# Kernel tuning notes

Measured on AMD Instinct MI355X. Metric: run time of the kernel, lower is better.

Reference implementation:

```python
import jax, jax.numpy as jnp
import numpy as np

B, T, C = 1, 4096, 1024
H = 16
D = C // H  # 64
LN_EPS = 1e-5


def layer_norm(x, g, b):
    mu = jnp.mean(x, axis=-1, keepdims=True)
    var = jnp.mean(jnp.square(x - mu), axis=-1, keepdims=True)
    return (x - mu) * jax.lax.rsqrt(var + LN_EPS) * g + b


def setup_inputs() -> dict:
    key = jax.random.key(0)
    ks = jax.random.split(key, 8)
    s = 0.02
    return {
        "x": jax.random.normal(ks[0], (B, T, C), dtype=jnp.float32),
        "ln1_g": jnp.ones((C,), jnp.float32),
        "ln1_b": jnp.zeros((C,), jnp.float32),
        "Wqkv": jax.random.normal(ks[1], (C, 3 * C), dtype=jnp.float32) * s,
        "bqkv": jnp.zeros((3 * C,), jnp.float32),
        "Wo": jax.random.normal(ks[2], (C, C), dtype=jnp.float32) * s,
        "bo": jnp.zeros((C,), jnp.float32),
        "ln2_g": jnp.ones((C,), jnp.float32),
        "ln2_b": jnp.zeros((C,), jnp.float32),
        "W1": jax.random.normal(ks[3], (C, 4 * C), dtype=jnp.float32) * s,
        "b1": jnp.zeros((4 * C,), jnp.float32),
        "W2": jax.random.normal(ks[4], (4 * C, C), dtype=jnp.float32) * s,
        "b2": jnp.zeros((C,), jnp.float32),
    }


def reference(x, ln1_g, ln1_b, Wqkv, bqkv, Wo, bo, ln2_g, ln2_b, W1, b1, W2, b2):
    b, t, c = x.shape
    x_norm = layer_norm(x, ln1_g, ln1_b)
    qkv = x_norm @ Wqkv + bqkv                      # [B,T,3C]
    qkv = qkv.reshape(b, t, 3, H, D).transpose(2, 0, 3, 1, 4)  # [3,B,H,T,D]
    Q, K, V = qkv[0], qkv[1], qkv[2]
    scores = jnp.einsum("bhtd,bhsd->bhts", Q, K) / jnp.sqrt(jnp.float32(D))
    causal = jnp.tril(jnp.ones((t, t), dtype=bool))  # [T,T]
    scores = jnp.where(causal[None, None], scores, -jnp.inf)
    weights = jax.nn.softmax(scores, axis=-1)
    attn = jnp.einsum("bhts,bhsd->bhtd", weights, V)  # [B,H,T,D]
    attn = attn.transpose(0, 2, 1, 3).reshape(b, t, c)
    x = x + (attn @ Wo + bo)
    h = layer_norm(x, ln2_g, ln2_b)
    h = jax.nn.gelu(h @ W1 + b1, approximate=False) @ W2 + b2
    return x + h
```

## Files before the change

kernel.cpp:

```cpp
#include <hip/hip_runtime.h>
#include <math.h>

typedef __bf16 bf16_t;
typedef __attribute__((ext_vector_type(8))) __bf16 bf16x8;
typedef __attribute__((ext_vector_type(4))) __bf16 bf16x4;
typedef __attribute__((ext_vector_type(4))) float f32x4;
typedef __attribute__((ext_vector_type(16))) float f32x16;
typedef __attribute__((ext_vector_type(4))) unsigned int u32x4;

#define T_LEN 4096
#define C_DIM 1024
#define NH 16
#define HD 64

__device__ __forceinline__ void gload_lds16(const void* g, void* l) {
    __builtin_amdgcn_global_load_lds(
        (__attribute__((address_space(1))) void*)(g),
        (__attribute__((address_space(3))) void*)(l), 16, 0, 0);
}

__device__ __forceinline__ f32x4 mfma16(bf16x8 a, bf16x8 b, f32x4 c) {
    return __builtin_amdgcn_mfma_f32_16x16x32_bf16(a, b, c, 0, 0, 0);
}

__device__ __forceinline__ f32x16 mfma32(bf16x8 a, bf16x8 b, f32x16 c) {
    return __builtin_amdgcn_mfma_f32_32x32x16_bf16(a, b, c, 0, 0, 0);
}

__device__ __forceinline__ float gelu_exact(float v) {
    return 0.5f * v * (1.0f + erff(v * 0.7071067811865476f));
}

__device__ __forceinline__ void make_frags2(const f32x16 s, bf16x8& fx, bf16x8& fy) {
    unsigned a0, a1, b0, b1;
    asm("v_cvt_pk_bf16_f32 %0, %1, %2" : "=v"(a0) : "v"(s[0]), "v"(s[1]));
    asm("v_cvt_pk_bf16_f32 %0, %1, %2" : "=v"(a1) : "v"(s[2]), "v"(s[3]));
    asm("v_cvt_pk_bf16_f32 %0, %1, %2" : "=v"(b0) : "v"(s[4]), "v"(s[5]));
    asm("v_cvt_pk_bf16_f32 %0, %1, %2" : "=v"(b1) : "v"(s[6]), "v"(s[7]));
    asm("v_permlane32_swap_b32 %0, %1" : "+v"(a0), "+v"(b0));
    asm("v_permlane32_swap_b32 %0, %1" : "+v"(a1), "+v"(b1));
    u32x4 wa = {a0, a1, b0, b1};
    fx = __builtin_bit_cast(bf16x8, wa);
    unsigned c0, c1, d0, d1;
    asm("v_cvt_pk_bf16_f32 %0, %1, %2" : "=v"(c0) : "v"(s[8]), "v"(s[9]));
    asm("v_cvt_pk_bf16_f32 %0, %1, %2" : "=v"(c1) : "v"(s[10]), "v"(s[11]));
    asm("v_cvt_pk_bf16_f32 %0, %1, %2" : "=v"(d0) : "v"(s[12]), "v"(s[13]));
    asm("v_cvt_pk_bf16_f32 %0, %1, %2" : "=v"(d1) : "v"(s[14]), "v"(s[15]));
    asm("v_permlane32_swap_b32 %0, %1" : "+v"(c0), "+v"(d0));
    asm("v_permlane32_swap_b32 %0, %1" : "+v"(c1), "+v"(d1));
    u32x4 wb = {c0, c1, d0, d1};
    fy = __builtin_bit_cast(bf16x8, wb);
}

__global__ __launch_bounds__(256) void transpose_all(
    const float* __restrict__ wqkv, const float* __restrict__ wo,
    const float* __restrict__ w1, const float* __restrict__ w2,
    bf16_t* __restrict__ oqkv, bf16_t* __restrict__ owo,
    bf16_t* __restrict__ ow1, bf16_t* __restrict__ ow2)
{
    __shared__ float tile[32][33];
    int s = blockIdx.x;
    const float* in; bf16_t* out; int R, C, NBX;
    if (s < 3072)      {            in = wqkv; out = oqkv; R = 1024; C = 3072; NBX = 96; }
    else if (s < 4096) { s -= 3072; in = wo;   out = owo;  R = 1024; C = 1024; NBX = 32; }
    else if (s < 8192) { s -= 4096; in = w1;   out = ow1;  R = 1024; C = 4096; NBX = 128; }
    else               { s -= 8192; in = w2;   out = ow2;  R = 4096; C = 1024; NBX = 32; }
    const int tx = threadIdx.x, ty = threadIdx.y;
    const int c0 = (s % NBX) * 32, r0 = (s / NBX) * 32;
#pragma unroll
    for (int j = 0; j < 4; ++j)
        tile[ty + j * 8][tx] = in[(size_t)(r0 + ty + j * 8) * C + c0 + tx];
    __syncthreads();
#pragma unroll
    for (int j = 0; j < 4; ++j)
        out[(size_t)(c0 + ty + j * 8) * R + r0 + tx] = (bf16_t)tile[tx][ty + j * 8];
}

__global__ __launch_bounds__(256) void ln_bf16(
    const float* __restrict__ x, const float* __restrict__ gam,
    const float* __restrict__ bet, bf16_t* __restrict__ out)
{
    const int row = blockIdx.x, t = threadIdx.x;
    const float4 v = *(const float4*)(x + (size_t)row * 1024 + t * 4);
    float s1 = v.x + v.y + v.z + v.w;
    float s2 = v.x * v.x + v.y * v.y + v.z * v.z + v.w * v.w;
#pragma unroll
    for (int m = 1; m < 64; m <<= 1) {
        s1 += __shfl_xor(s1, m);
        s2 += __shfl_xor(s2, m);
    }
    __shared__ float red[8];
    if ((t & 63) == 0) { red[(t >> 6) * 2] = s1; red[(t >> 6) * 2 + 1] = s2; }
    __syncthreads();
    s1 = red[0] + red[2] + red[4] + red[6];
    s2 = red[1] + red[3] + red[5] + red[7];
    const float mu = s1 * (1.0f / 1024.0f);
    const float inv = rsqrtf(s2 * (1.0f / 1024.0f) - mu * mu + 1e-5f);
    const float4 gg = *(const float4*)(gam + t * 4);
    const float4 bb = *(const float4*)(bet + t * 4);
    bf16x4 o;
    o[0] = (bf16_t)((v.x - mu) * inv * gg.x + bb.x);
    o[1] = (bf16_t)((v.y - mu) * inv * gg.y + bb.y);
    o[2] = (bf16_t)((v.z - mu) * inv * gg.z + bb.z);
    o[3] = (bf16_t)((v.w - mu) * inv * gg.w + bb.w);
    *(bf16x4*)(out + (size_t)row * 1024 + t * 4) = o;
}

template <int EPI>
__global__ __launch_bounds__(256, 2) void gemm_bt(
    const bf16_t* __restrict__ A, const bf16_t* __restrict__ Bt,
    const float* __restrict__ bias, const float* __restrict__ res,
    bf16_t* __restrict__ outb, float* __restrict__ outf,
    int M, int N, int Klen, int Kstr)
{
    __shared__ alignas(1024) bf16_t Alds[4][128 * 32];
    __shared__ alignas(1024) bf16_t Blds[4][128 * 32];
    const int t = threadIdx.x;
    const int lane = t & 63, w = t >> 6;
    const int wr = w >> 1, wc = w & 1;
    const int g = lane >> 4, ci = lane & 15;

    const int NB = gridDim.x, MB = gridDim.y;
    const int flat = blockIdx.x + NB * blockIdx.y;
    const int xcd = flat & 7, slot = flat >> 3;
    const int by = xcd * (MB >> 3) + slot / NB;
    const int bx = slot % NB;
    const int m0 = by * 128, n0 = bx * 128;

    f32x4 acc[4][4];
#pragma unroll
    for (int i = 0; i < 4; ++i)
#pragma unroll
        for (int j = 0; j < 4; ++j)
#pragma unroll
            for (int k = 0; k < 4; ++k) acc[i][j][k] = 0.0f;

    const int r0 = t >> 2;
    const int cc = (t & 3) * 8;
    const int nkt = Klen >> 5;

    auto stage = [&](int kt) {
        const int b = kt & 3;
        const int kk = kt * 32;
        char* aB = (char*)&Alds[b][0] + w * 1024;
        char* bB = (char*)&Blds[b][0] + w * 1024;
        gload_lds16(A + (size_t)(m0 + r0) * Kstr + kk + cc, aB);
        gload_lds16(A + (size_t)(m0 + r0 + 64) * Kstr + kk + cc, aB + 4096);
        gload_lds16(Bt + (size_t)(n0 + r0) * Kstr + kk + cc, bB);
        gload_lds16(Bt + (size_t)(n0 + r0 + 64) * Kstr + kk + cc, bB + 4096);
    };

    stage(0);
    if (nkt > 1) stage(1);
    for (int kt = 0; kt < nkt; ++kt) {
        if (kt + 2 < nkt) {
            stage(kt + 2);
            asm volatile("s_waitcnt vmcnt(8)" ::: "memory");
        } else if (kt + 1 < nkt) {
            asm volatile("s_waitcnt vmcnt(4)" ::: "memory");
        } else {
            asm volatile("s_waitcnt vmcnt(0)" ::: "memory");
        }
        __builtin_amdgcn_s_barrier();
        __builtin_amdgcn_sched_barrier(0);
        const int b = kt & 3;
        const bf16_t* ap = &Alds[b][0] + (wr * 64 + ci) * 32 + g * 8;
        const bf16_t* bp = &Blds[b][0] + (wc * 64 + ci) * 32 + g * 8;
        bf16x8 af[4], bf[4];
#pragma unroll
        for (int mt = 0; mt < 4; ++mt) af[mt] = *(const bf16x8*)(ap + mt * 16 * 32);
#pragma unroll
        for (int nt = 0; nt < 4; ++nt) bf[nt] = *(const bf16x8*)(bp + nt * 16 * 32);
        __builtin_amdgcn_s_setprio(1);
#pragma unroll
        for (int mt = 0; mt < 4; ++mt)
#pragma unroll
            for (int nt = 0; nt < 4; ++nt)
                acc[mt][nt] = mfma16(af[mt], bf[nt], acc[mt][nt]);
        __builtin_amdgcn_s_setprio(0);
    }

#pragma unroll
    for (int nt = 0; nt < 4; ++nt) {
        const int col = n0 + wc * 64 + nt * 16 + ci;
        const float bv = bias[col];
#pragma unroll
        for (int mt = 0; mt < 4; ++mt) {
            const int row = m0 + wr * 64 + mt * 16 + g * 4;
#pragma unroll
            for (int r = 0; r < 4; ++r) {
                float v = acc[mt][nt][r] + bv;
                if constexpr (EPI == 1) v = gelu_exact(v);
                if constexpr (EPI == 2) {
                    outf[(size_t)(row + r) * N + col] =
                        v + res[(size_t)(row + r) * N + col];
                } else {
                    outb[(size_t)(row + r) * N + col] = (bf16_t)v;
                }
            }
        }
    }
}

__global__ __launch_bounds__(512, 1) void gemm_w2(
    const bf16_t* __restrict__ A, const bf16_t* __restrict__ Bt,
    const float* __restrict__ bias, const float* __restrict__ res,
    float* __restrict__ out, int M, int N, int Khalf, int Kstr)
{
    __shared__ alignas(1024) char smem[131072];
    bf16_t* ring = (bf16_t*)smem;
    const int t = threadIdx.x;
    const int grp = t >> 8, tl = t & 255;
    const int lane = tl & 63, w = tl >> 6;
    const int wr = w >> 1, wc = w & 1;
    const int g = lane >> 4, ci = lane & 15;

    const int NB = gridDim.x, MB = gridDim.y;
    const int flat = blockIdx.x + NB * blockIdx.y;
    const int xcd = flat & 7, slot = flat >> 3;
    const int by = xcd * (MB >> 3) + slot / NB;
    const int bx = slot % NB;
    const int m0 = by * 128, n0 = bx * 128;

    const bf16_t* Ag = A + (size_t)grp * Khalf;
    const bf16_t* Bg = Bt + (size_t)grp * Khalf;

    f32x4 acc[4][4];
#pragma unroll
    for (int i = 0; i < 4; ++i)
#pragma unroll
        for (int j = 0; j < 4; ++j)
#pragma unroll
            for (int k = 0; k < 4; ++k) acc[i][j][k] = 0.0f;

    const int r0 = tl >> 2;
    const int cc = (tl & 3) * 8;
    const int nkt = Khalf >> 5;

    auto stage = [&](int kt) {
        const int b = kt & 3;
        const int kk = kt * 32;
        bf16_t* base = ring + grp * 32768 + b * 8192;
        char* aB = (char*)base + w * 1024;
        char* bB = (char*)(base + 4096) + w * 1024;
        gload_lds16(Ag + (size_t)(m0 + r0) * Kstr + kk + cc, aB);
        gload_lds16(Ag + (size_t)(m0 + r0 + 64) * Kstr + kk + cc, aB + 4096);
        gload_lds16(Bg + (size_t)(n0 + r0) * Kstr + kk + cc, bB);
        gload_lds16(Bg + (size_t)(n0 + r0 + 64) * Kstr + kk + cc, bB + 4096);
    };

    stage(0);
    stage(1);
    for (int kt = 0; kt < nkt; ++kt) {
        if (kt + 2 < nkt) {
            stage(kt + 2);
            asm volatile("s_waitcnt vmcnt(8)" ::: "memory");
        } else if (kt + 1 < nkt) {
            asm volatile("s_waitcnt vmcnt(4)" ::: "memory");
        } else {
            asm volatile("s_waitcnt vmcnt(0)" ::: "memory");
        }
        __builtin_amdgcn_s_barrier();
        __builtin_amdgcn_sched_barrier(0);
        const bf16_t* base = ring + grp * 32768 + (kt & 3) * 8192;
        const bf16_t* ap = base + (wr * 64 + ci) * 32 + g * 8;
        const bf16_t* bp = base + 4096 + (wc * 64 + ci) * 32 + g * 8;
        bf16x8 af[4], bf[4];
#pragma unroll
        for (int mt = 0; mt < 4; ++mt) af[mt] = *(const bf16x8*)(ap + mt * 16 * 32);
#pragma unroll
        for (int nt = 0; nt < 4; ++nt) bf[nt] = *(const bf16x8*)(bp + nt * 16 * 32);
        __builtin_amdgcn_s_setprio(1);
#pragma unroll
        for (int mt = 0; mt < 4; ++mt)
#pragma unroll
            for (int nt = 0; nt < 4; ++nt)
                acc[mt][nt] = mfma16(af[mt], bf[nt], acc[mt][nt]);
        __builtin_amdgcn_s_setprio(0);
    }

    __syncthreads();
    float* ex = (float*)smem;
    if (grp == 1) {
#pragma unroll
        for (int mt = 0; mt < 4; ++mt)
#pragma unroll
            for (int nt = 0; nt < 4; ++nt)
                *(f32x4*)(ex + tl * 68 + (mt * 4 + nt) * 4) = acc[mt][nt];
    }
    __syncthreads();
    if (grp == 0) {
#pragma unroll
        for (int nt = 0; nt < 4; ++nt) {
            const int col = n0 + wc * 64 + nt * 16 + ci;
            const float bv = bias[col];
#pragma unroll
            for (int mt = 0; mt < 4; ++mt) {
                const int row = m0 + wr * 64 + mt * 16 + g * 4;
                const f32x4 p1 = *(const f32x4*)(ex + tl * 68 + (mt * 4 + nt) * 4);
#pragma unroll
                for (int r = 0; r < 4; ++r) {
                    out[(size_t)(row + r) * N + col] =
                        acc[mt][nt][r] + p1[r] + bv +
                        res[(size_t)(row + r) * N + col];
                }
            }
        }
    }
}

template <int EPI>
__global__ __launch_bounds__(512, 2) void gemm256(
    const bf16_t* __restrict__ A, const bf16_t* __restrict__ Bt,
    const float* __restrict__ bias, bf16_t* __restrict__ outb,
    bf16_t* __restrict__ vtout, int M, int N, int K)
{
    __shared__ alignas(1024) bf16_t lds[2][2][256 * 64];
    const int t = threadIdx.x, lane = t & 63, w = t >> 6;
    const int g = lane >> 4, ci = lane & 15;
    const int wr = w >> 2, wc = w & 3;
    const int NB = gridDim.x;
    const int nwg = NB * gridDim.y;
    const int flat = blockIdx.x + NB * blockIdx.y;
    const int rix = (flat & 7) * (nwg >> 3) + (flat >> 3);
    const int m0 = (rix / NB) * 256, n0 = (rix % NB) * 256;
    const int NKT = K >> 6;

    f32x4 acc[8][4];
#pragma unroll
    for (int i = 0; i < 8; ++i)
#pragma unroll
        for (int j = 0; j < 4; ++j)
#pragma unroll
            for (int k2 = 0; k2 < 4; ++k2) acc[i][j][k2] = 0.0f;

    const int sw0 = (g ^ (ci & 7)) * 8;
    const int sw1 = ((4 + g) ^ (ci & 7)) * 8;

    auto stage = [&](int h, int ktile, int b) {
#pragma unroll
        for (int i = 0; i < 2; ++i) {
            const int idx = i * 512 + t;
            const int r = idx >> 3;
            const int c = (t & 7) ^ (r & 7);
            const bf16_t* src = ((h < 2) ? A : Bt)
                + (size_t)(((h < 2) ? m0 : n0) + (h & 1) * 128 + r) * K
                + ktile * 64 + c * 8;
            bf16_t* dst = &lds[b][h >> 1][(h & 1) * 8192] + (i * 512 + w * 64) * 8;
            gload_lds16(src, dst);
        }
    };

    bf16x8 a[4][2], b2[2][2][2];

    stage(0, 0, 0); stage(3, 0, 0); stage(1, 0, 0); stage(2, 0, 0);
    if (NKT > 1) { stage(0, 1, 1); stage(3, 1, 1); stage(1, 1, 1); }
    asm volatile("s_waitcnt vmcnt(6)" ::: "memory");
    __builtin_amdgcn_s_barrier();

    for (int kt = 0; kt < NKT; ++kt) {
        const int cur = kt & 1;
        const bf16_t* Ab = &lds[cur][0][0];
        const bf16_t* Bb = &lds[cur][1][0];

#pragma unroll
        for (int mi = 0; mi < 4; ++mi) {
            const bf16_t* ap = Ab + (wr * 64 + mi * 16 + ci) * 64;
            a[mi][0] = *(const bf16x8*)(ap + sw0);
            a[mi][1] = *(const bf16x8*)(ap + sw1);
        }
#pragma unroll
        for (int ni = 0; ni < 2; ++ni) {
            const bf16_t* bp = Bb + (wc * 32 + ni * 16 + ci) * 64;
            b2[0][ni][0] = *(const bf16x8*)(bp + sw0);
            b2[0][ni][1] = *(const bf16x8*)(bp + sw1);
        }
        if (kt + 1 < NKT) stage(2, kt + 1, cur ^ 1);
        __builtin_amdgcn_s_barrier();
        asm volatile("s_waitcnt lgkmcnt(0)" ::: "memory");
        __builtin_amdgcn_sched_barrier(0);
        __builtin_amdgcn_s_setprio(1);
#pragma unroll
        for (int mi = 0; mi < 4; ++mi)
#pragma unroll
            for (int ni = 0; ni < 2; ++ni) {
                acc[mi][ni] = mfma16(a[mi][0], b2[0][ni][0], acc[mi][ni]);
                acc[mi][ni] = mfma16(a[mi][1], b2[0][ni][1], acc[mi][ni]);
            }
        __builtin_amdgcn_s_setprio(0);
        __builtin_amdgcn_s_barrier();

#pragma unroll
        for (int ni = 0; ni < 2; ++ni) {
            const bf16_t* bp = Bb + (128 + wc * 32 + ni * 16 + ci) * 64;
            b2[1][ni][0] = *(const bf16x8*)(bp + sw0);
            b2[1][ni][1] = *(const bf16x8*)(bp + sw1);
        }
        if (kt + 2 < NKT) stage(0, kt + 2, cur);
        __builtin_amdgcn_s_barrier();
        asm volatile("s_waitcnt lgkmcnt(0)" ::: "memory");
        __builtin_amdgcn_sched_barrier(0);
        __builtin_amdgcn_s_setprio(1);
#pragma unroll
        for (int mi = 0; mi < 4; ++mi)
#pragma unroll
            for (int ni = 0; ni < 2; ++ni) {
                acc[mi][2 + ni] = mfma16(a[mi][0], b2[1][ni][0], acc[mi][2 + ni]);
                acc[mi][2 + ni] = mfma16(a[mi][1], b2[1][ni][1], acc[mi][2 + ni]);
            }
        __builtin_amdgcn_s_setprio(0);
        __builtin_amdgcn_s_barrier();

#pragma unroll
        for (int mi = 0; mi < 4; ++mi) {
            const bf16_t* ap = Ab + (128 + wr * 64 + mi * 16 + ci) * 64;
            a[mi][0] = *(const bf16x8*)(ap + sw0);
            a[mi][1] = *(const bf16x8*)(ap + sw1);
        }
        if (kt + 2 < NKT) stage(3, kt + 2, cur);
        __builtin_amdgcn_s_barrier();
        asm volatile("s_waitcnt lgkmcnt(0)" ::: "memory");
        __builtin_amdgcn_sched_barrier(0);
        __builtin_amdgcn_s_setprio(1);
#pragma unroll
        for (int mi = 0; mi < 4; ++mi)
#pragma unroll
            for (int ni = 0; ni < 2; ++ni) {
                acc[4 + mi][2 + ni] = mfma16(a[mi][0], b2[1][ni][0], acc[4 + mi][2 + ni]);
                acc[4 + mi][2 + ni] = mfma16(a[mi][1], b2[1][ni][1], acc[4 + mi][2 + ni]);
            }
        __builtin_amdgcn_s_setprio(0);
        __builtin_amdgcn_s_barrier();

        if (kt + 2 < NKT) stage(1, kt + 2, cur);
        __builtin_amdgcn_s_barrier();
        __builtin_amdgcn_s_setprio(1);
#pragma unroll
        for (int mi = 0; mi < 4; ++mi)
#pragma unroll
            for (int ni = 0; ni < 2; ++ni) {
                acc[4 + mi][ni] = mfma16(a[mi][0], b2[0][ni][0], acc[4 + mi][ni]);
                acc[4 + mi][ni] = mfma16(a[mi][1], b2[0][ni][1], acc[4 + mi][ni]);
            }
        __builtin_amdgcn_s_setprio(0);
        if (kt + 2 < NKT) asm volatile("s_waitcnt vmcnt(6)" ::: "memory");
        else              asm volatile("s_waitcnt vmcnt(0)" ::: "memory");
        __builtin_amdgcn_s_barrier();
    }

    const float QSC = 0.125f * 1.4426950408889634f;
#pragma unroll
    for (int mrep = 0; mrep < 8; ++mrep) {
        const int row = m0 + (mrep >> 2) * 128 + wr * 64 + (mrep & 3) * 16 + g * 4;
#pragma unroll
        for (int nrep = 0; nrep < 4; ++nrep) {
            const int col = n0 + (nrep >> 1) * 128 + wc * 32 + (nrep & 1) * 16 + ci;
            const float bv = bias[col];
            if (EPI == 2 && col >= 2048) {
                const int cv = col - 2048;
                bf16x4 o4;
#pragma unroll
                for (int jr = 0; jr < 4; ++jr)
                    o4[jr] = (bf16_t)(acc[mrep][nrep][jr] + bv);
                *(bf16x4*)(vtout + (size_t)(cv >> 6) * 262144
                           + (size_t)(cv & 63) * 4096 + row) = o4;
            } else {
                const float sc = (EPI == 2 && col < 1024) ? QSC : 1.0f;
#pragma unroll
                for (int jr = 0; jr < 4; ++jr) {
                    float v = acc[mrep][nrep][jr] + bv;
                    if constexpr (EPI == 1) v = gelu_exact(v);
                    if (EPI == 2) v *= sc;
                    outb[(size_t)(row + jr) * N + col] = (bf16_t)v;
                }
            }
        }
    }
}

__global__ __launch_bounds__(256, 2) void attn_fwd(
    const bf16_t* __restrict__ qkv, const bf16_t* __restrict__ vt,
    bf16_t* __restrict__ opart, float* __restrict__ lbuf)
{
    __shared__ alignas(1024) bf16_t Klds[2][64 * 64];
    __shared__ alignas(1024) bf16_t Vlds[2][64 * 64];
    const int t = threadIdx.x, lane = t & 63, w = t >> 6;
    const int hi = lane >> 5, li = lane & 31;
    const int lq = li >> 2;
    const int h = blockIdx.x;
    const int y = blockIdx.y;
    const int qt = 31 - (y >> 1);
    const int chunk = y & 1;
    const int q0 = qt * 128;
    const int qrow = q0 + w * 32 + li;
    const int wDiag = 2 * qt + (w >> 1);
    const int ktA = chunk ? (qt + 1) : 0;
    const int ktB = chunk ? (2 * qt + 2) : (qt + 1);

    bf16x8 qf[4];
#pragma unroll
    for (int ks = 0; ks < 4; ++ks)
        qf[ks] = *(const bf16x8*)(qkv + (size_t)qrow * 3072 + h * 64 + ks * 16 + hi * 8);
    bf16x8 ones8;
#pragma unroll
    for (int j = 0; j < 8; ++j) ones8[j] = (bf16_t)1.0f;

    f32x16 oacc[2], lacc;
#pragma unroll
    for (int r = 0; r < 16; ++r) { oacc[0][r] = 0.0f; oacc[1][r] = 0.0f; lacc[r] = 0.0f; }

    const int sr = t >> 3;
    const int sx = ((t & 7) ^ ((sr >> 2) & 7)) * 8;

    auto stageKV = [&](int kt, int b) {
        const size_t kbase = (size_t)(kt * 64) * 3072 + 1024 + h * 64 + sx;
        const size_t vbase = (size_t)h * 262144 + (size_t)kt * 64 + sx;
#pragma unroll
        for (int i = 0; i < 2; ++i) {
            gload_lds16(qkv + kbase + (size_t)(i * 32 + sr) * 3072,
                        (char*)&Klds[b][0] + (size_t)(i * 2048 + t * 8) * 2);
            gload_lds16(vt + vbase + (size_t)(i * 32 + sr) * 4096,
                        (char*)&Vlds[b][0] + (size_t)(i * 2048 + t * 8) * 2);
        }
    };

    stageKV(ktA, 0);
    for (int kt = ktA; kt < ktB; ++kt) {
        const int cur = (kt - ktA) & 1;
        asm volatile("s_waitcnt vmcnt(0)" ::: "memory");
        __syncthreads();
        if (kt + 1 < ktB) stageKV(kt + 1, cur ^ 1);

        if (kt <= wDiag) {
            const bf16_t* Kb = &Klds[cur][0];
            const bf16_t* Vb = &Vlds[cur][0];
            f32x16 s0, s1;
#pragma unroll
            for (int r = 0; r < 16; ++r) { s0[r] = 0.0f; s1[r] = 0.0f; }

            __builtin_amdgcn_s_setprio(1);
#pragma unroll
            for (int ks = 0; ks < 4; ++ks) {
                const int cs = ((ks * 2 + hi) ^ lq) * 8;
                s0 = mfma32(*(const bf16x8*)(Kb + li * 64 + cs), qf[ks], s0);
                s1 = mfma32(*(const bf16x8*)(Kb + (32 + li) * 64 + cs), qf[ks], s1);
            }
            __builtin_amdgcn_s_setprio(0);

            bf16x8 vf[4][2];
#pragma unroll
            for (int ks = 0; ks < 4; ++ks) {
                const int cs = ((ks * 2 + hi) ^ lq) * 8;
                vf[ks][0] = *(const bf16x8*)(Vb + li * 64 + cs);
                vf[ks][1] = *(const bf16x8*)(Vb + (32 + li) * 64 + cs);
            }

            if (kt == wDiag) {
                const int kb0 = kt * 64 + 4 * hi;
#pragma unroll
                for (int r = 0; r < 16; ++r) {
                    const int kp0 = kb0 + (r & 3) + 8 * (r >> 2);
                    if (kp0 > qrow) s0[r] = -1e30f;
                    if (kp0 + 32 > qrow) s1[r] = -1e30f;
                }
            }
#pragma unroll
            for (int r = 0; r < 16; ++r) {
                s0[r] = exp2f(s0[r]);
                s1[r] = exp2f(s1[r]);
            }

            bf16x8 pf[4];
            make_frags2(s0, pf[0], pf[1]);
            make_frags2(s1, pf[2], pf[3]);

            __builtin_amdgcn_s_setprio(1);
#pragma unroll
            for (int ks = 0; ks < 4; ++ks) {
                oacc[0] = mfma32(vf[ks][0], pf[ks], oacc[0]);
                oacc[1] = mfma32(vf[ks][1], pf[ks], oacc[1]);
                lacc    = mfma32(ones8,     pf[ks], lacc);
            }
            __builtin_amdgcn_s_setprio(0);
        }
        __syncthreads();
    }

    bf16_t* op = opart + ((size_t)chunk * T_LEN + qrow) * 1024 + h * 64 + hi * 4;
#pragma unroll
    for (int dblk = 0; dblk < 2; ++dblk)
#pragma unroll
        for (int gi = 0; gi < 4; ++gi) {
            bf16x4 o4;
#pragma unroll
            for (int j = 0; j < 4; ++j) o4[j] = (bf16_t)oacc[dblk][gi * 4 + j];
            *(bf16x4*)(op + dblk * 32 + gi * 8) = o4;
        }
    if (hi == 0)
        lbuf[((size_t)chunk * T_LEN + qrow) * NH + h] = lacc[0];
}

__global__ __launch_bounds__(256) void attn_combine(
    const bf16_t* __restrict__ opart, const float* __restrict__ lbuf,
    bf16_t* __restrict__ out)
{
    const int row = blockIdx.x, t = threadIdx.x;
    const int c = t * 4, h = c >> 6;
    const float l0 = lbuf[(size_t)row * NH + h];
    const float l1 = lbuf[((size_t)T_LEN + row) * NH + h];
    const float inv = 1.0f / (l0 + l1);
    const bf16x4 o0 = *(const bf16x4*)(opart + (size_t)row * 1024 + c);
    const bf16x4 o1 = *(const bf16x4*)(opart + ((size_t)T_LEN + row) * 1024 + c);
    bf16x4 o;
#pragma unroll
    for (int j = 0; j < 4; ++j)
        o[j] = (bf16_t)(((float)o0[j] + (float)o1[j]) * inv);
    *(bf16x4*)(out + (size_t)row * 1024 + c) = o;
}

extern "C" void kernel_launch(void* const* d_in, const int* in_sizes, int n_in,
                              void* d_out, int out_size, void* d_ws, size_t ws_size,
                              hipStream_t stream)
{
    const float* x    = (const float*)d_in[0];
    const float* ln1g = (const float*)d_in[1];
    const float* ln1b = (const float*)d_in[2];
    const float* Wqkv = (const float*)d_in[3];
    const float* bqkv = (const float*)d_in[4];
    const float* Wo   = (const float*)d_in[5];
    const float* bo   = (const float*)d_in[6];
    const float* ln2g = (const float*)d_in[7];
    const float* ln2b = (const float*)d_in[8];
    const float* W1   = (const float*)d_in[9];
    const float* b1   = (const float*)d_in[10];
    const float* W2   = (const float*)d_in[11];
    const float* b2   = (const float*)d_in[12];
    float* outp = (float*)d_out;

    char* p = (char*)d_ws;
    bf16_t* WqkvT = (bf16_t*)p; p += (size_t)3072 * 1024 * 2;
    bf16_t* WoT   = (bf16_t*)p; p += (size_t)1024 * 1024 * 2;
    bf16_t* W1T   = (bf16_t*)p; p += (size_t)4096 * 1024 * 2;
    bf16_t* W2T   = (bf16_t*)p; p += (size_t)1024 * 4096 * 2;
    bf16_t* xn    = (bf16_t*)p; p += (size_t)4096 * 1024 * 2;
    bf16_t* qkv   = (bf16_t*)p; p += (size_t)4096 * 3072 * 2;
    bf16_t* vtb   = (bf16_t*)p; p += (size_t)16 * 64 * 4096 * 2;
    bf16_t* attnb = (bf16_t*)p; p += (size_t)4096 * 1024 * 2;
    float*  x2    = (float*)p;  p += (size_t)4096 * 1024 * 4;
    bf16_t* hb    = (bf16_t*)p; p += (size_t)4096 * 1024 * 2;
    bf16_t* g1    = (bf16_t*)p; p += (size_t)4096 * 4096 * 2;
    bf16_t* opart = (bf16_t*)p; p += (size_t)2 * 4096 * 1024 * 2;
    float*  lbuf  = (float*)p;  p += (size_t)2 * 4096 * 16 * 4;

    transpose_all<<<12288, dim3(32, 8), 0, stream>>>(Wqkv, Wo, W1, W2,
                                                     WqkvT, WoT, W1T, W2T);

    ln_bf16<<<4096, 256, 0, stream>>>(x, ln1g, ln1b, xn);
    gemm256<2><<<dim3(12, 16), 512, 0, stream>>>(xn, WqkvT, bqkv,
                                                 qkv, vtb, 4096, 3072, 1024);
    attn_fwd<<<dim3(16, 64), 256, 0, stream>>>(qkv, vtb, opart, lbuf);
    attn_combine<<<4096, 256, 0, stream>>>(opart, lbuf, attnb);
    gemm_bt<2><<<dim3(8, 32), 256, 0, stream>>>(attnb, WoT, bo, x,
                                                nullptr, x2, 4096, 1024, 1024, 1024);
    ln_bf16<<<4096, 256, 0, stream>>>(x2, ln2g, ln2b, hb);
    gemm256<1><<<dim3(16, 16), 512, 0, stream>>>(hb, W1T, b1,
                                                 g1, nullptr, 4096, 4096, 1024);
    gemm_w2<<<dim3(8, 32), 512, 0, stream>>>(g1, W2T, b2, x2,
                                             outp, 4096, 1024, 2048, 4096);
}
```

Baseline: 246.1 us.

## Use 256-row query tiles with four KV chunks and route Wo GEMM through split-K kernel

```diff
diff --git a/kernel.cpp b/kernel.cpp
--- a/kernel.cpp
+++ b/kernel.cpp
@@ -106,102 +106,6 @@
     *(bf16x4*)(out + (size_t)row * 1024 + t * 4) = o;
 }
 
-template <int EPI>
-__global__ __launch_bounds__(256, 2) void gemm_bt(
-    const bf16_t* __restrict__ A, const bf16_t* __restrict__ Bt,
-    const float* __restrict__ bias, const float* __restrict__ res,
-    bf16_t* __restrict__ outb, float* __restrict__ outf,
-    int M, int N, int Klen, int Kstr)
-{
-    __shared__ alignas(1024) bf16_t Alds[4][128 * 32];
-    __shared__ alignas(1024) bf16_t Blds[4][128 * 32];
-    const int t = threadIdx.x;
-    const int lane = t & 63, w = t >> 6;
-    const int wr = w >> 1, wc = w & 1;
-    const int g = lane >> 4, ci = lane & 15;
-
-    const int NB = gridDim.x, MB = gridDim.y;
-    const int flat = blockIdx.x + NB * blockIdx.y;
-    const int xcd = flat & 7, slot = flat >> 3;
-    const int by = xcd * (MB >> 3) + slot / NB;
-    const int bx = slot % NB;
-    const int m0 = by * 128, n0 = bx * 128;
-
-    f32x4 acc[4][4];
-#pragma unroll
-    for (int i = 0; i < 4; ++i)
-#pragma unroll
-        for (int j = 0; j < 4; ++j)
-#pragma unroll
-            for (int k = 0; k < 4; ++k) acc[i][j][k] = 0.0f;
-
-    const int r0 = t >> 2;
-    const int cc = (t & 3) * 8;
-    const int nkt = Klen >> 5;
-
-    auto stage = [&](int kt) {
-        const int b = kt & 3;
-        const int kk = kt * 32;
-        char* aB = (char*)&Alds[b][0] + w * 1024;
-        char* bB = (char*)&Blds[b][0] + w * 1024;
-        gload_lds16(A + (size_t)(m0 + r0) * Kstr + kk + cc, aB);
-        gload_lds16(A + (size_t)(m0 + r0 + 64) * Kstr + kk + cc, aB + 4096);
-        gload_lds16(Bt + (size_t)(n0 + r0) * Kstr + kk + cc, bB);
-        gload_lds16(Bt + (size_t)(n0 + r0 + 64) * Kstr + kk + cc, bB + 4096);
-    };
-
-    stage(0);
-    if (nkt > 1) stage(1);
-    for (int kt = 0; kt < nkt; ++kt) {
-        if (kt + 2 < nkt) {
-            stage(kt + 2);
-            asm volatile("s_waitcnt vmcnt(8)" ::: "memory");
-        } else if (kt + 1 < nkt) {
-            asm volatile("s_waitcnt vmcnt(4)" ::: "memory");
-        } else {
-            asm volatile("s_waitcnt vmcnt(0)" ::: "memory");
-        }
-        __builtin_amdgcn_s_barrier();
-        __builtin_amdgcn_sched_barrier(0);
-        const int b = kt & 3;
-        const bf16_t* ap = &Alds[b][0] + (wr * 64 + ci) * 32 + g * 8;
-        const bf16_t* bp = &Blds[b][0] + (wc * 64 + ci) * 32 + g * 8;
-        bf16x8 af[4], bf[4];
-#pragma unroll
-        for (int mt = 0; mt < 4; ++mt) af[mt] = *(const bf16x8*)(ap + mt * 16 * 32);
-#pragma unroll
-        for (int nt = 0; nt < 4; ++nt) bf[nt] = *(const bf16x8*)(bp + nt * 16 * 32);
-        __builtin_amdgcn_s_setprio(1);
-#pragma unroll
-        for (int mt = 0; mt < 4; ++mt)
-#pragma unroll
-            for (int nt = 0; nt < 4; ++nt)
-                acc[mt][nt] = mfma16(af[mt], bf[nt], acc[mt][nt]);
-        __builtin_amdgcn_s_setprio(0);
-    }
-
-#pragma unroll
-    for (int nt = 0; nt < 4; ++nt) {
-        const int col = n0 + wc * 64 + nt * 16 + ci;
-        const float bv = bias[col];
-#pragma unroll
-        for (int mt = 0; mt < 4; ++mt) {
-            const int row = m0 + wr * 64 + mt * 16 + g * 4;
-#pragma unroll
-            for (int r = 0; r < 4; ++r) {
-                float v = acc[mt][nt][r] + bv;
-                if constexpr (EPI == 1) v = gelu_exact(v);
-                if constexpr (EPI == 2) {
-                    outf[(size_t)(row + r) * N + col] =
-                        v + res[(size_t)(row + r) * N + col];
-                } else {
-                    outb[(size_t)(row + r) * N + col] = (bf16_t)v;
-                }
-            }
-        }
-    }
-}
-
 __global__ __launch_bounds__(512, 1) void gemm_w2(
     const bf16_t* __restrict__ A, const bf16_t* __restrict__ Bt,
     const float* __restrict__ bias, const float* __restrict__ res,
@@ -478,7 +382,7 @@
     }
 }
 
-__global__ __launch_bounds__(256, 2) void attn_fwd(
+__global__ __launch_bounds__(512, 2) void attn_fwd(
     const bf16_t* __restrict__ qkv, const bf16_t* __restrict__ vt,
     bf16_t* __restrict__ opart, float* __restrict__ lbuf)
 {
@@ -489,13 +393,13 @@
     const int lq = li >> 2;
     const int h = blockIdx.x;
     const int y = blockIdx.y;
-    const int qt = 31 - (y >> 1);
-    const int chunk = y & 1;
-    const int q0 = qt * 128;
+    const int qt = 15 - (y >> 2);
+    const int chunk = y & 3;
+    const int q0 = qt * 256;
     const int qrow = q0 + w * 32 + li;
-    const int wDiag = 2 * qt + (w >> 1);
-    const int ktA = chunk ? (qt + 1) : 0;
-    const int ktB = chunk ? (2 * qt + 2) : (qt + 1);
+    const int wDiag = 4 * qt + (w >> 1);
+    const int ktA = chunk * (qt + 1);
+    const int ktB = ktA + qt + 1;
 
     bf16x8 qf[4];
 #pragma unroll
@@ -513,15 +417,10 @@
     const int sx = ((t & 7) ^ ((sr >> 2) & 7)) * 8;
 
     auto stageKV = [&](int kt, int b) {
-        const size_t kbase = (size_t)(kt * 64) * 3072 + 1024 + h * 64 + sx;
-        const size_t vbase = (size_t)h * 262144 + (size_t)kt * 64 + sx;
-#pragma unroll
-        for (int i = 0; i < 2; ++i) {
-            gload_lds16(qkv + kbase + (size_t)(i * 32 + sr) * 3072,
-                        (char*)&Klds[b][0] + (size_t)(i * 2048 + t * 8) * 2);
-            gload_lds16(vt + vbase + (size_t)(i * 32 + sr) * 4096,
-                        (char*)&Vlds[b][0] + (size_t)(i * 2048 + t * 8) * 2);
-        }
+        gload_lds16(qkv + (size_t)(kt * 64 + sr) * 3072 + 1024 + h * 64 + sx,
+                    (char*)&Klds[b][0] + (size_t)t * 16);
+        gload_lds16(vt + (size_t)h * 262144 + (size_t)sr * 4096 + kt * 64 + sx,
+                    (char*)&Vlds[b][0] + (size_t)t * 16);
     };
 
     stageKV(ktA, 0);
@@ -606,15 +505,21 @@
 {
     const int row = blockIdx.x, t = threadIdx.x;
     const int c = t * 4, h = c >> 6;
-    const float l0 = lbuf[(size_t)row * NH + h];
-    const float l1 = lbuf[((size_t)T_LEN + row) * NH + h];
-    const float inv = 1.0f / (l0 + l1);
-    const bf16x4 o0 = *(const bf16x4*)(opart + (size_t)row * 1024 + c);
-    const bf16x4 o1 = *(const bf16x4*)(opart + ((size_t)T_LEN + row) * 1024 + c);
+    float l = 0.0f;
+#pragma unroll
+    for (int k = 0; k < 4; ++k)
+        l += lbuf[((size_t)k * T_LEN + row) * NH + h];
+    const float inv = 1.0f / l;
+    float acc4[4] = {0.f, 0.f, 0.f, 0.f};
+#pragma unroll
+    for (int k = 0; k < 4; ++k) {
+        const bf16x4 o = *(const bf16x4*)(opart + ((size_t)k * T_LEN + row) * 1024 + c);
+#pragma unroll
+        for (int j = 0; j < 4; ++j) acc4[j] += (float)o[j];
+    }
     bf16x4 o;
 #pragma unroll
-    for (int j = 0; j < 4; ++j)
-        o[j] = (bf16_t)(((float)o0[j] + (float)o1[j]) * inv);
+    for (int j = 0; j < 4; ++j) o[j] = (bf16_t)(acc4[j] * inv);
     *(bf16x4*)(out + (size_t)row * 1024 + c) = o;
 }
 
@@ -649,8 +554,8 @@
     float*  x2    = (float*)p;  p += (size_t)4096 * 1024 * 4;
     bf16_t* hb    = (bf16_t*)p; p += (size_t)4096 * 1024 * 2;
     bf16_t* g1    = (bf16_t*)p; p += (size_t)4096 * 4096 * 2;
-    bf16_t* opart = (bf16_t*)p; p += (size_t)2 * 4096 * 1024 * 2;
-    float*  lbuf  = (float*)p;  p += (size_t)2 * 4096 * 16 * 4;
+    bf16_t* opart = (bf16_t*)p; p += (size_t)4 * 4096 * 1024 * 2;
+    float*  lbuf  = (float*)p;  p += (size_t)4 * 4096 * 16 * 4;
 
     transpose_all<<<12288, dim3(32, 8), 0, stream>>>(Wqkv, Wo, W1, W2,
                                                      WqkvT, WoT, W1T, W2T);
@@ -658,10 +563,10 @@
     ln_bf16<<<4096, 256, 0, stream>>>(x, ln1g, ln1b, xn);
     gemm256<2><<<dim3(12, 16), 512, 0, stream>>>(xn, WqkvT, bqkv,
                                                  qkv, vtb, 4096, 3072, 1024);
-    attn_fwd<<<dim3(16, 64), 256, 0, stream>>>(qkv, vtb, opart, lbuf);
+    attn_fwd<<<dim3(16, 64), 512, 0, stream>>>(qkv, vtb, opart, lbuf);
     attn_combine<<<4096, 256, 0, stream>>>(opart, lbuf, attnb);
-    gemm_bt<2><<<dim3(8, 32), 256, 0, stream>>>(attnb, WoT, bo, x,
-                                                nullptr, x2, 4096, 1024, 1024, 1024);
+    gemm_w2<<<dim3(8, 32), 512, 0, stream>>>(attnb, WoT, bo, x,
+                                             x2, 4096, 1024, 512, 1024);
     ln_bf16<<<4096, 256, 0, stream>>>(x2, ln2g, ln2b, hb);
     gemm256<1><<<dim3(16, 16), 512, 0, stream>>>(hb, W1T, b1,
                                                  g1, nullptr, 4096, 4096, 1024);
```

Result: slower. 258.2 us (+4.9%).
